# Performance work log

Measured on AMD Instinct MI355X. Metric: run time of the kernel, lower is better.

## Reference

```python
import jax, jax.numpy as jnp
import numpy as np

STRIDE = 1

def setup_inputs() -> dict:
    key = jax.random.key(0)
    k1, k2, k3 = jax.random.split(key, 3)
    bs, pep_len, d = 2048, 15, 64
    out_channels, kernel_size, mhc_len = 128, 9, 34
    peptide_x = jax.random.normal(k1, (bs, pep_len, d), dtype=jnp.float32)
    mhc_x = jax.random.normal(k2, (bs, mhc_len, d), dtype=jnp.float32)
    weight = jax.random.normal(k3, (out_channels, kernel_size, mhc_len), dtype=jnp.float32) * 0.02
    bias = jnp.zeros((out_channels,), dtype=jnp.float32)
    return {"peptide_x": peptide_x, "mhc_x": mhc_x, "weight": weight, "bias": bias}

def reference(peptide_x, mhc_x, weight, bias):
    # kernel[n,o,d,k] = relu(sum_l mhc_x[n,l,d] * weight[o,k,l])
    kernel = jax.nn.relu(jnp.einsum('nld,okl->nodk', mhc_x, weight))
    bs, pep_len, d = peptide_x.shape
    ksize = kernel.shape[-1]
    L_out = (pep_len - ksize) // STRIDE + 1
    # sliding windows: [bs, L_out, k, d]
    idx = jnp.arange(L_out)[:, None] * STRIDE + jnp.arange(ksize)[None, :]
    windows = peptide_x[:, idx, :]
    # grouped conv1d (groups=bs) == per-sample contraction over (d, k)
    out = jnp.einsum('ntkd,nodk->not', windows, kernel)
    return out + bias[:, None]
```

## Files before the change

kernel.cpp:

```cpp
#include <hip/hip_runtime.h>

typedef __attribute__((ext_vector_type(8))) short bf16x8;
typedef __attribute__((ext_vector_type(4))) float f32x4;
typedef unsigned short ushort_t;
typedef unsigned int uint_t;

constexpr int PEP = 15;
constexpr int D   = 64;
constexpr int L   = 34;
constexpr int OC  = 128;
constexpr int KS  = 9;
constexpr int TO  = 7;
constexpr int OK  = OC * KS;
constexpr int MTG = OK / 16;
constexpr int NCH = 8;
constexpr int NCHB = 4;
constexpr int CHO = OC / NCH;
constexpr int MT_CH = (CHO * KS) / 16;
constexpr int CTS = 145;
constexpr int SOS = CHO * TO;
constexpr int WPN = 2 * MTG * 2 * 64 * 8;
constexpr int SMEM_BYTES = 64 * CTS * 4 + 4 * SOS * 4;

__device__ __forceinline__ ushort_t f2bf(float v) {
    uint_t u = __float_as_uint(v);
    return (ushort_t)((u + 0x7fffu + ((u >> 16) & 1u)) >> 16);
}
__device__ __forceinline__ float bf2f(ushort_t h) {
    return __uint_as_float(((uint_t)h) << 16);
}

template <int CTRL>
__device__ __forceinline__ float dpp_shr_add(float v) {
    int x = __builtin_amdgcn_update_dpp(0, __float_as_int(v), CTRL, 0xF, 0xF, true);
    return v + __int_as_float(x);
}

__global__ void wprep_kernel(const float* __restrict__ W, ushort_t* __restrict__ wp) {
    int x = blockIdx.x * 256 + threadIdx.x;
    if (x >= WPN) return;
    int i  = x & 7;
    int ln = (x >> 3) & 63;
    int ks = (x >> 9) & 1;
    int mt = (x >> 10) % MTG;
    int sp = x / (MTG * 1024);
    int ok = mt * 16 + (ln & 15);
    int l  = (ln >> 4) * 8 + i + 32 * ks;
    float v = (l < L) ? W[ok * L + l] : 0.0f;
    ushort_t hi = f2bf(v);
    if (sp == 0) wp[x] = hi;
    else         wp[x] = f2bf(v - bf2f(hi));
}

__global__ __launch_bounds__(256, 3) void iconv_mfma(
    const float* __restrict__ pep,
    const float* __restrict__ mhc,
    const ushort_t* __restrict__ wp,
    const float* __restrict__ bias,
    float* __restrict__ out)
{
    __shared__ __align__(16) char smem[SMEM_BYTES];
    const int n    = blockIdx.x;
    const int c0   = blockIdx.y * NCHB;
    const int tid  = threadIdx.x;
    const int lane = tid & 63;
    const int w    = tid >> 6;

    float p[PEP];
    {
        const float* pp = pep + (size_t)n * PEP * D + lane;
        #pragma unroll
        for (int j = 0; j < PEP; ++j) p[j] = pp[j * D];
    }

    {
        const float* mp = mhc + (size_t)n * L * D + lane;
        #pragma unroll
        for (int j = 0; j < 16; ++j) {
            int l = w + 4 * j;
            float v = (l < L) ? mp[l * D] : 0.0f;
            ushort_t hi = f2bf(v);
            ushort_t lo = f2bf(v - bf2f(hi));
            int byte = (lane * 128 + l * 2) ^ ((lane & 7) << 4);
            *(ushort_t*)(smem + byte)        = hi;
            *(ushort_t*)(smem + 8192 + byte) = lo;
        }
    }
    __syncthreads();

    bf16x8 bf[4][2][2];
    #pragma unroll
    for (int nt = 0; nt < 4; ++nt) {
        int d = (lane & 15) + 16 * nt;
        #pragma unroll
        for (int ks = 0; ks < 2; ++ks) {
            int l0 = (lane >> 4) * 8 + 32 * ks;
            int byte = (d * 128 + l0 * 2) ^ ((d & 7) << 4);
            bf[nt][ks][0] = *(const bf16x8*)(smem + byte);
            bf[nt][ks][1] = *(const bf16x8*)(smem + 8192 + byte);
        }
    }
    __syncthreads();

    float* CT  = (float*)smem;
    float* so  = (float*)(smem + 64 * CTS * 4);
    float* CTl = CT + lane * CTS;

    auto do_tile = [&](int cg, int mtl) {
        const ushort_t* base = wp + (size_t)(cg * MT_CH + mtl) * 1024 + lane * 8;
        bf16x8 ah0 = *(const bf16x8*)(base);
        bf16x8 ah1 = *(const bf16x8*)(base + 512);
        bf16x8 al0 = *(const bf16x8*)(base + MTG * 1024);
        bf16x8 al1 = *(const bf16x8*)(base + MTG * 1024 + 512);

        f32x4 acc[4];
        #pragma unroll
        for (int nt = 0; nt < 4; ++nt) acc[nt] = (f32x4){0.f, 0.f, 0.f, 0.f};
        #pragma unroll
        for (int nt = 0; nt < 4; ++nt) {
            acc[nt] = __builtin_amdgcn_mfma_f32_16x16x32_bf16(ah0, bf[nt][0][0], acc[nt], 0, 0, 0);
            acc[nt] = __builtin_amdgcn_mfma_f32_16x16x32_bf16(ah1, bf[nt][1][0], acc[nt], 0, 0, 0);
            acc[nt] = __builtin_amdgcn_mfma_f32_16x16x32_bf16(ah0, bf[nt][0][1], acc[nt], 0, 0, 0);
            acc[nt] = __builtin_amdgcn_mfma_f32_16x16x32_bf16(ah1, bf[nt][1][1], acc[nt], 0, 0, 0);
            acc[nt] = __builtin_amdgcn_mfma_f32_16x16x32_bf16(al0, bf[nt][0][0], acc[nt], 0, 0, 0);
            acc[nt] = __builtin_amdgcn_mfma_f32_16x16x32_bf16(al1, bf[nt][1][0], acc[nt], 0, 0, 0);
        }

        int r0 = mtl * 16 + (lane >> 4) * 4;
        #pragma unroll
        for (int nt = 0; nt < 4; ++nt) {
            int d = (lane & 15) + 16 * nt;
            float* dst = CT + d * CTS + r0;
            dst[0] = fmaxf(acc[nt][0], 0.f);
            dst[1] = fmaxf(acc[nt][1], 0.f);
            dst[2] = fmaxf(acc[nt][2], 0.f);
            dst[3] = fmaxf(acc[nt][3], 0.f);
        }
    };

    for (int c = 0; c < NCHB; ++c) {
        const int cg = c0 + c;

        do_tile(cg, w);
        do_tile(cg, w + 4);
        if (w == (cg & 3)) do_tile(cg, 8);
        __syncthreads();

        #pragma unroll
        for (int h = 0; h < 2; ++h) {
            float a2[2][TO];
            #pragma unroll
            for (int oi = 0; oi < 2; ++oi)
                #pragma unroll
                for (int t = 0; t < TO; ++t) a2[oi][t] = 0.f;

            #pragma unroll
            for (int oi = 0; oi < 2; ++oi) {
                const float* row = CTl + (w * 4 + h * 2 + oi) * KS;
                #pragma unroll
                for (int k = 0; k < KS; ++k) {
                    float kk = row[k];
                    #pragma unroll
                    for (int t = 0; t < TO; ++t) a2[oi][t] = fmaf(kk, p[t + k], a2[oi][t]);
                }
            }

            #pragma unroll
            for (int oi = 0; oi < 2; ++oi) {
                #pragma unroll
                for (int t = 0; t < TO; ++t) {
                    float a = a2[oi][t];
                    a = dpp_shr_add<0x111>(a);
                    a = dpp_shr_add<0x112>(a);
                    a = dpp_shr_add<0x114>(a);
                    a = dpp_shr_add<0x118>(a);
                    if ((lane & 15) == 15)
                        so[(lane >> 4) * SOS + (w * 4 + h * 2 + oi) * TO + t] = a;
                }
            }
        }
        __syncthreads();

        if (tid < SOS) {
            int o = cg * CHO + tid / TO;
            float v = (so[tid] + so[SOS + tid]) +
                      (so[2 * SOS + tid] + so[3 * SOS + tid]);
            out[(size_t)n * OC * TO + cg * SOS + tid] = v + bias[o];
        }
    }
}

__global__ __launch_bounds__(256, 4) void iconv_f32(
    const float* __restrict__ pep, const float* __restrict__ mhc,
    const float* __restrict__ wsrc, const float* __restrict__ bias,
    float* __restrict__ out)
{
    __shared__ float so[4 * 900];
    const int n = blockIdx.x, tid = threadIdx.x, lane = tid & 63;
    const int w = __builtin_amdgcn_readfirstlane(tid >> 6);
    float m[L];
    { const float* mp = mhc + (size_t)n * L * D + lane;
      #pragma unroll
      for (int l = 0; l < L; ++l) m[l] = mp[l * D]; }
    float p[PEP];
    { const float* pp = pep + (size_t)n * PEP * D + lane;
      #pragma unroll
      for (int j = 0; j < PEP; ++j) p[j] = pp[j * D]; }
    for (int oo = 0; oo < OC / 4; ++oo) {
        const int o = w * (OC / 4) + oo;
        float acc[TO];
        #pragma unroll
        for (int t = 0; t < TO; ++t) acc[t] = 0.f;
        #pragma unroll
        for (int k = 0; k < KS; ++k) {
            const float2* wrow = reinterpret_cast<const float2*>(wsrc + (size_t)o * KS * L);
            float wr[L];
            #pragma unroll
            for (int q = 0; q < L / 2; ++q) {
                float2 v = wrow[k * (L / 2) + q];
                wr[q * 2] = v.x; wr[q * 2 + 1] = v.y;
            }
            float k0 = 0.f, k1 = 0.f, k2 = 0.f, k3 = 0.f;
            #pragma unroll
            for (int l = 0; l < 32; l += 4) {
                k0 = fmaf(m[l], wr[l], k0);   k1 = fmaf(m[l + 1], wr[l + 1], k1);
                k2 = fmaf(m[l + 2], wr[l + 2], k2); k3 = fmaf(m[l + 3], wr[l + 3], k3);
            }
            k0 = fmaf(m[32], wr[32], k0); k1 = fmaf(m[33], wr[33], k1);
            float kk = fmaxf((k0 + k2) + (k1 + k3), 0.f);
            #pragma unroll
            for (int t = 0; t < TO; ++t) acc[t] = fmaf(p[t + k], kk, acc[t]);
        }
        #pragma unroll
        for (int t = 0; t < TO; ++t) {
            float a = acc[t];
            a += __shfl_xor(a, 1, 64); a += __shfl_xor(a, 2, 64);
            a += __shfl_xor(a, 4, 64); a += __shfl_xor(a, 8, 64);
            if ((lane & 15) == 0) so[(lane >> 4) * 900 + o * TO + t] = a;
        }
    }
    __syncthreads();
    float* on = out + (size_t)n * OC * TO;
    for (int i = tid; i < OC * TO; i += 256) {
        int o = i / TO;
        on[i] = (so[i] + so[900 + i]) + (so[1800 + i] + so[2700 + i]) + bias[o];
    }
}

extern "C" void kernel_launch(void* const* d_in, const int* in_sizes, int n_in,
                              void* d_out, int out_size, void* d_ws, size_t ws_size,
                              hipStream_t stream) {
    const float* pep  = (const float*)d_in[0];
    const float* mhc  = (const float*)d_in[1];
    const float* W    = (const float*)d_in[2];
    const float* bias = (const float*)d_in[3];
    float* out        = (float*)d_out;
    const int bs = in_sizes[0] / (PEP * D);

    const size_t need = (size_t)WPN * sizeof(ushort_t);
    if (d_ws != nullptr && ws_size >= need) {
        ushort_t* wpx = (ushort_t*)d_ws;
        wprep_kernel<<<(WPN + 255) / 256, 256, 0, stream>>>(W, wpx);
        iconv_mfma<<<dim3(bs, 2), 256, 0, stream>>>(pep, mhc, wpx, bias, out);
    } else {
        iconv_f32<<<bs, 256, 0, stream>>>(pep, mhc, W, bias, out);
    }
}
```

Measured before the change: 169.6 us.

## Split L=34 contraction into 32-wide MFMA plus fp32 FMA tail

The 34-long contraction was padded to 64 and run as two K=32 MFMA steps per split-bf16 product. Now only the first 32 l values go through MFMA (3 MFMAs per n-tile instead of 6), and the last two l values are added with fp32 FMAs using a separate fp32 weight tail and per-lane mhc values. This roughly halves MFMA work and B-fragment registers, and the launch bounds are raised to target 4 blocks per CU. It adds extra global loads for the tail weights and a different workspace layout.

```diff
diff --git a/kernel.cpp b/kernel.cpp
--- a/kernel.cpp
+++ b/kernel.cpp
@@ -19,7 +19,8 @@
 constexpr int MT_CH = (CHO * KS) / 16;
 constexpr int CTS = 145;
 constexpr int SOS = CHO * TO;
-constexpr int WPN = 2 * MTG * 2 * 64 * 8;
+constexpr int WP_FRAG = 36864;
+constexpr int WP_TAILF = 36864;
 constexpr int SMEM_BYTES = 64 * CTS * 4 + 4 * SOS * 4;
 
 __device__ __forceinline__ ushort_t f2bf(float v) {
@@ -38,21 +39,29 @@
 
 __global__ void wprep_kernel(const float* __restrict__ W, ushort_t* __restrict__ wp) {
     int x = blockIdx.x * 256 + threadIdx.x;
-    if (x >= WPN) return;
-    int i  = x & 7;
-    int ln = (x >> 3) & 63;
-    int ks = (x >> 9) & 1;
-    int mt = (x >> 10) % MTG;
-    int sp = x / (MTG * 1024);
-    int ok = mt * 16 + (ln & 15);
-    int l  = (ln >> 4) * 8 + i + 32 * ks;
-    float v = (l < L) ? W[ok * L + l] : 0.0f;
-    ushort_t hi = f2bf(v);
-    if (sp == 0) wp[x] = hi;
-    else         wp[x] = f2bf(v - bf2f(hi));
-}
-
-__global__ __launch_bounds__(256, 3) void iconv_mfma(
+    if (x < 2 * WP_FRAG) {
+        int sp = x / WP_FRAG;
+        int r  = x % WP_FRAG;
+        int i  = r & 7;
+        int ln = (r >> 3) & 63;
+        int mt = r >> 9;
+        int ok = mt * 16 + (ln & 15);
+        int l  = (ln >> 4) * 8 + i;
+        float v = W[ok * L + l];
+        ushort_t hi = f2bf(v);
+        wp[x] = sp ? f2bf(v - bf2f(hi)) : hi;
+    } else if (x < 2 * WP_FRAG + WP_TAILF) {
+        int y  = x - 2 * WP_FRAG;
+        int c  = y & 1;
+        int j  = (y >> 1) & 3;
+        int ln = (y >> 3) & 63;
+        int mt = y >> 9;
+        int row = mt * 16 + (ln >> 4) * 4 + j;
+        ((float*)(wp + 2 * WP_FRAG))[y] = W[row * L + 32 + c];
+    }
+}
+
+__global__ __launch_bounds__(256, 4) void iconv_mfma(
     const float* __restrict__ pep,
     const float* __restrict__ mhc,
     const ushort_t* __restrict__ wp,
@@ -73,12 +82,23 @@
         for (int j = 0; j < PEP; ++j) p[j] = pp[j * D];
     }
 
+    float m32v[4], m33v[4];
+    {
+        const float* mb = mhc + (size_t)n * L * D;
+        #pragma unroll
+        for (int nt = 0; nt < 4; ++nt) {
+            int d = (lane & 15) + 16 * nt;
+            m32v[nt] = mb[32 * D + d];
+            m33v[nt] = mb[33 * D + d];
+        }
+    }
+
     {
         const float* mp = mhc + (size_t)n * L * D + lane;
         #pragma unroll
-        for (int j = 0; j < 16; ++j) {
+        for (int j = 0; j < 8; ++j) {
             int l = w + 4 * j;
-            float v = (l < L) ? mp[l * D] : 0.0f;
+            float v = mp[l * D];
             ushort_t hi = f2bf(v);
             ushort_t lo = f2bf(v - bf2f(hi));
             int byte = (lane * 128 + l * 2) ^ ((lane & 7) << 4);
@@ -88,42 +108,46 @@
     }
     __syncthreads();
 
-    bf16x8 bf[4][2][2];
+    bf16x8 bf[4][2];
     #pragma unroll
     for (int nt = 0; nt < 4; ++nt) {
         int d = (lane & 15) + 16 * nt;
-        #pragma unroll
-        for (int ks = 0; ks < 2; ++ks) {
-            int l0 = (lane >> 4) * 8 + 32 * ks;
-            int byte = (d * 128 + l0 * 2) ^ ((d & 7) << 4);
-            bf[nt][ks][0] = *(const bf16x8*)(smem + byte);
-            bf[nt][ks][1] = *(const bf16x8*)(smem + 8192 + byte);
-        }
+        int l0 = (lane >> 4) * 8;
+        int byte = (d * 128 + l0 * 2) ^ ((d & 7) << 4);
+        bf[nt][0] = *(const bf16x8*)(smem + byte);
+        bf[nt][1] = *(const bf16x8*)(smem + 8192 + byte);
     }
     __syncthreads();
 
     float* CT  = (float*)smem;
     float* so  = (float*)(smem + 64 * CTS * 4);
     float* CTl = CT + lane * CTS;
+    const float* wtail = (const float*)(wp + 2 * WP_FRAG);
 
     auto do_tile = [&](int cg, int mtl) {
-        const ushort_t* base = wp + (size_t)(cg * MT_CH + mtl) * 1024 + lane * 8;
-        bf16x8 ah0 = *(const bf16x8*)(base);
-        bf16x8 ah1 = *(const bf16x8*)(base + 512);
-        bf16x8 al0 = *(const bf16x8*)(base + MTG * 1024);
-        bf16x8 al1 = *(const bf16x8*)(base + MTG * 1024 + 512);
+        int mtG = cg * MT_CH + mtl;
+        const ushort_t* base = wp + mtG * 512 + lane * 8;
+        bf16x8 ah = *(const bf16x8*)(base);
+        bf16x8 al = *(const bf16x8*)(base + WP_FRAG);
+        const float4* tb = (const float4*)(wtail + (size_t)(mtG * 64 + lane) * 8);
+        float4 ft0 = tb[0];
+        float4 ft1 = tb[1];
 
         f32x4 acc[4];
         #pragma unroll
         for (int nt = 0; nt < 4; ++nt) acc[nt] = (f32x4){0.f, 0.f, 0.f, 0.f};
         #pragma unroll
         for (int nt = 0; nt < 4; ++nt) {
-            acc[nt] = __builtin_amdgcn_mfma_f32_16x16x32_bf16(ah0, bf[nt][0][0], acc[nt], 0, 0, 0);
-            acc[nt] = __builtin_amdgcn_mfma_f32_16x16x32_bf16(ah1, bf[nt][1][0], acc[nt], 0, 0, 0);
-            acc[nt] = __builtin_amdgcn_mfma_f32_16x16x32_bf16(ah0, bf[nt][0][1], acc[nt], 0, 0, 0);
-            acc[nt] = __builtin_amdgcn_mfma_f32_16x16x32_bf16(ah1, bf[nt][1][1], acc[nt], 0, 0, 0);
-            acc[nt] = __builtin_amdgcn_mfma_f32_16x16x32_bf16(al0, bf[nt][0][0], acc[nt], 0, 0, 0);
-            acc[nt] = __builtin_amdgcn_mfma_f32_16x16x32_bf16(al1, bf[nt][1][0], acc[nt], 0, 0, 0);
+            acc[nt] = __builtin_amdgcn_mfma_f32_16x16x32_bf16(ah, bf[nt][0], acc[nt], 0, 0, 0);
+            acc[nt] = __builtin_amdgcn_mfma_f32_16x16x32_bf16(ah, bf[nt][1], acc[nt], 0, 0, 0);
+            acc[nt] = __builtin_amdgcn_mfma_f32_16x16x32_bf16(al, bf[nt][0], acc[nt], 0, 0, 0);
+        }
+        #pragma unroll
+        for (int nt = 0; nt < 4; ++nt) {
+            acc[nt][0] = fmaf(ft0.x, m32v[nt], fmaf(ft0.y, m33v[nt], acc[nt][0]));
+            acc[nt][1] = fmaf(ft0.z, m32v[nt], fmaf(ft0.w, m33v[nt], acc[nt][1]));
+            acc[nt][2] = fmaf(ft1.x, m32v[nt], fmaf(ft1.y, m33v[nt], acc[nt][2]));
+            acc[nt][3] = fmaf(ft1.z, m32v[nt], fmaf(ft1.w, m33v[nt], acc[nt][3]));
         }
 
         int r0 = mtl * 16 + (lane >> 4) * 4;
@@ -257,10 +281,11 @@
     float* out        = (float*)d_out;
     const int bs = in_sizes[0] / (PEP * D);
 
-    const size_t need = (size_t)WPN * sizeof(ushort_t);
+    const size_t need = 2 * WP_FRAG * sizeof(ushort_t) + WP_TAILF * sizeof(float);
     if (d_ws != nullptr && ws_size >= need) {
         ushort_t* wpx = (ushort_t*)d_ws;
-        wprep_kernel<<<(WPN + 255) / 256, 256, 0, stream>>>(W, wpx);
+        const int tot = 2 * WP_FRAG + WP_TAILF;
+        wprep_kernel<<<(tot + 255) / 256, 256, 0, stream>>>(W, wpx);
         iconv_mfma<<<dim3(bs, 2), 256, 0, stream>>>(pep, mhc, wpx, bias, out);
     } else {
         iconv_f32<<<bs, 256, 0, stream>>>(pep, mhc, W, bias, out);
```

Result: faster. 150.3 us (-11.4%).
